# Optimization experiments

Measured on AMD Instinct MI355X. Metric: run time of the kernel, lower is better.

## Reference

```python
import jax, jax.numpy as jnp
import numpy as np

NEG = -9e15
EPS = 1e-5

def setup_inputs() -> dict:
    key = jax.random.key(0)
    k1, k2, k3, k4 = jax.random.split(key, 4)
    B, S, D = 4, 2048, 1024
    q = jax.random.normal(k1, (B, S, D), dtype=jnp.float32)
    k = jax.random.normal(k2, (B, S, D), dtype=jnp.float32)
    v = jax.random.normal(k3, (B, S, D), dtype=jnp.float32)
    mask = jax.random.randint(k4, (B, S, S), 0, 2, dtype=jnp.int32)
    gamma = jnp.ones((D,), dtype=jnp.float32)
    beta = jnp.zeros((D,), dtype=jnp.float32)
    return {"q": q, "k": k, "v": v, "mask": mask, "gamma": gamma, "beta": beta}

def reference(q, k, v, mask, gamma, beta):
    d_k = q.shape[-1]
    # scaled dot-product attention: [B,S,S] logits materialized as in original
    logits = jnp.einsum('bsd,btd->bst', q, k) / jnp.sqrt(jnp.asarray(d_k, q.dtype))
    logits = jnp.where(mask == 0, jnp.asarray(NEG, logits.dtype), logits)
    attn = jax.nn.softmax(logits, axis=-1)
    x = jnp.einsum('bst,btd->bsd', attn, v)
    # dropout is identity at inference; LayerNorm over last dim
    mu = jnp.mean(x, axis=-1, keepdims=True)
    var = jnp.mean(jnp.square(x - mu), axis=-1, keepdims=True)
    xhat = (x - mu) * jax.lax.rsqrt(var + EPS)
    return xhat * gamma + beta
```

## Files before the change

kernel.cpp:

```cpp
#include <hip/hip_runtime.h>
#include <hip/hip_bf16.h>

typedef unsigned short u16;
typedef __attribute__((ext_vector_type(8))) short bf16x8;
typedef __attribute__((ext_vector_type(4))) float f32x4;
typedef __attribute__((ext_vector_type(4))) float float4v;
typedef __attribute__((ext_vector_type(4))) short short4v;

#define BB 4
#define SS 2048
#define DD 1024

__device__ __forceinline__ u16 f2bf(float x){
    unsigned u = __float_as_uint(x);
    return (u16)((u + 0x7fffu + ((u >> 16) & 1u)) >> 16);
}

#define GLD16(g, l) __builtin_amdgcn_global_load_lds( \
    (const __attribute__((address_space(1))) unsigned int*)(g), \
    (__attribute__((address_space(3))) unsigned int*)(l), 16, 0, 0)

__global__ void conv_bf16_kernel(const float* __restrict__ in,
                                 u16* __restrict__ out, int n4, float scale){
    int i = blockIdx.x * 256 + threadIdx.x;
    if (i >= n4) return;
    float4v v = ((const float4v*)in)[i];
    short4v o;
    o[0] = (short)f2bf(v[0] * scale); o[1] = (short)f2bf(v[1] * scale);
    o[2] = (short)f2bf(v[2] * scale); o[3] = (short)f2bf(v[3] * scale);
    ((short4v*)out)[i] = o;
}

__global__ void transpose_v_kernel(const float* __restrict__ v,
                                   u16* __restrict__ vt){
    __shared__ float tile[64][65];
    const int b  = blockIdx.z;
    const int s0 = blockIdx.x << 6;
    const int d0 = blockIdx.y << 6;
    const int tx = threadIdx.x & 15;
    const int ty = threadIdx.x >> 4;
#pragma unroll
    for (int kk = 0; kk < 4; ++kk){
        const float* p = v + ((b * SS + s0 + ty + 16 * kk) * DD) + d0 + tx * 4;
        float4v val = *(const float4v*)p;
        tile[ty + 16 * kk][tx * 4 + 0] = val[0];
        tile[ty + 16 * kk][tx * 4 + 1] = val[1];
        tile[ty + 16 * kk][tx * 4 + 2] = val[2];
        tile[ty + 16 * kk][tx * 4 + 3] = val[3];
    }
    __syncthreads();
#pragma unroll
    for (int kk = 0; kk < 4; ++kk){
        int dy = ty + 16 * kk;
        short4v o;
        o[0] = (short)f2bf(tile[tx * 4 + 0][dy]);
        o[1] = (short)f2bf(tile[tx * 4 + 1][dy]);
        o[2] = (short)f2bf(tile[tx * 4 + 2][dy]);
        o[3] = (short)f2bf(tile[tx * 4 + 3][dy]);
        *(short4v*)&vt[((b * DD + d0 + dy) * SS) + s0 + tx * 4] = o;
    }
}

__global__ void zero_f32(float* __restrict__ p, int n){
    int i = blockIdx.x * 256 + threadIdx.x;
    if (i < n) p[i] = 0.f;
}

__global__ __launch_bounds__(256, 4) void qk_kernel(
    const u16* __restrict__ Qb, const u16* __restrict__ Kb,
    const int* __restrict__ mask, u16* __restrict__ P,
    float* __restrict__ rowsum)
{
    __shared__ __align__(16) u16 Abuf[2][128 * 32];
    __shared__ __align__(16) u16 Bbuf[2][128 * 32];
    __shared__ float rsred[2][128];

    const int flat = blockIdx.x;
    const int swz  = (flat & 7) * 128 + (flat >> 3);
    const int bx = swz & 15, by = (swz >> 4) & 15, b = swz >> 8;

    const int tid  = threadIdx.x;
    const int wid  = tid >> 6, lane = tid & 63;
    const int l16  = lane & 15, g4 = lane >> 4;
    const int wr   = wid >> 1,  wc = wid & 1;
    const int row0 = bx << 7;
    const int col0 = by << 7;

    f32x4 acc[4][4];
    const f32x4 z4 = {0.f, 0.f, 0.f, 0.f};
#pragma unroll
    for (int i = 0; i < 4; ++i)
#pragma unroll
        for (int j = 0; j < 4; ++j) acc[i][j] = z4;

    const int off0 = wid * 1024 + lane * 16;
    const int ar0  = off0 >> 6;
    const int ac0  = (off0 & 63) >> 1;
    const int ldso = wid * 1024 + lane * 16;

    const u16* gQ = Qb + ((size_t)(b * SS + row0 + ar0)) * DD + ac0;
    const u16* gK = Kb + ((size_t)(b * SS + col0 + ar0)) * DD + ac0;

#define QK_STAGE(t, bi) { \
    GLD16(gQ + (t) * 32,            (char*)Abuf[bi] + ldso); \
    GLD16(gQ + 64 * DD + (t) * 32,  (char*)Abuf[bi] + 4096 + ldso); \
    GLD16(gK + (t) * 32,            (char*)Bbuf[bi] + ldso); \
    GLD16(gK + 64 * DD + (t) * 32,  (char*)Bbuf[bi] + 4096 + ldso); }

    QK_STAGE(0, 0);
    __syncthreads();

    const int NT = DD / 32;
    for (int t = 0; t < NT; ++t){
        const int cur = t & 1;
        if (t + 1 < NT) QK_STAGE(t + 1, cur ^ 1);
        bf16x8 af[4], bfr[4];
#pragma unroll
        for (int i = 0; i < 4; ++i){
            af[i]  = *(const bf16x8*)&Abuf[cur][(wr * 64 + i * 16 + l16) * 32 + g4 * 8];
            bfr[i] = *(const bf16x8*)&Bbuf[cur][(wc * 64 + i * 16 + l16) * 32 + g4 * 8];
        }
#pragma unroll
        for (int i = 0; i < 4; ++i)
#pragma unroll
            for (int j = 0; j < 4; ++j)
                acc[i][j] = __builtin_amdgcn_mfma_f32_16x16x32_bf16(af[i], bfr[j], acc[i][j], 0, 0, 0);
        __syncthreads();
    }
#undef QK_STAGE

    float rs[4][4];
#pragma unroll
    for (int i = 0; i < 4; ++i)
#pragma unroll
        for (int r = 0; r < 4; ++r) rs[i][r] = 0.f;

#pragma unroll
    for (int i = 0; i < 4; ++i){
#pragma unroll
        for (int j = 0; j < 4; ++j){
#pragma unroll
            for (int r = 0; r < 4; ++r){
                const int grow = row0 + wr * 64 + i * 16 + g4 * 4 + r;
                const int gcol = col0 + wc * 64 + j * 16 + l16;
                const size_t idx = ((size_t)(b * SS + grow)) * SS + gcol;
                int m = mask[idx];
                float e = m ? __expf(acc[i][j][r]) : 0.f;
                P[idx] = f2bf(e);
                rs[i][r] += e;
            }
        }
    }
#pragma unroll
    for (int i = 0; i < 4; ++i)
#pragma unroll
        for (int r = 0; r < 4; ++r){
            float v = rs[i][r];
            v += __shfl_xor(v, 1); v += __shfl_xor(v, 2);
            v += __shfl_xor(v, 4); v += __shfl_xor(v, 8);
            if (l16 == 0) rsred[wc][wr * 64 + i * 16 + g4 * 4 + r] = v;
        }
    __syncthreads();
    if (tid < 128)
        atomicAdd(&rowsum[b * SS + row0 + tid], rsred[0][tid] + rsred[1][tid]);
}

__global__ __launch_bounds__(256, 4) void pv_kernel(
    const u16* __restrict__ P, const u16* __restrict__ Vt,
    const float* __restrict__ rowsum, u16* __restrict__ Xn)
{
    __shared__ __align__(16) u16 Abuf[2][128 * 32];
    __shared__ __align__(16) u16 Bbuf[2][128 * 32];

    const int flat = blockIdx.x;
    const int swz  = (flat & 7) * 64 + (flat >> 3);
    const int bx = swz & 15, by = (swz >> 4) & 7, b = swz >> 7;

    const int tid  = threadIdx.x;
    const int wid  = tid >> 6, lane = tid & 63;
    const int l16  = lane & 15, g4 = lane >> 4;
    const int wr   = wid >> 1,  wc = wid & 1;
    const int row0 = bx << 7;
    const int col0 = by << 7;

    f32x4 acc[4][4];
    const f32x4 z4 = {0.f, 0.f, 0.f, 0.f};
#pragma unroll
    for (int i = 0; i < 4; ++i)
#pragma unroll
        for (int j = 0; j < 4; ++j) acc[i][j] = z4;

    const int off0 = wid * 1024 + lane * 16;
    const int ar0  = off0 >> 6;
    const int ac0  = (off0 & 63) >> 1;
    const int ldso = wid * 1024 + lane * 16;

    const u16* gP = P  + ((size_t)(b * SS + row0 + ar0)) * SS + ac0;
    const u16* gV = Vt + ((size_t)(b * DD + col0 + ar0)) * SS + ac0;

#define PV_STAGE(t, bi) { \
    GLD16(gP + (t) * 32,            (char*)Abuf[bi] + ldso); \
    GLD16(gP + 64 * SS + (t) * 32,  (char*)Abuf[bi] + 4096 + ldso); \
    GLD16(gV + (t) * 32,            (char*)Bbuf[bi] + ldso); \
    GLD16(gV + 64 * SS + (t) * 32,  (char*)Bbuf[bi] + 4096 + ldso); }

    PV_STAGE(0, 0);
    __syncthreads();

    const int NT = SS / 32;
    for (int t = 0; t < NT; ++t){
        const int cur = t & 1;
        if (t + 1 < NT) PV_STAGE(t + 1, cur ^ 1);
        bf16x8 af[4], bfr[4];
#pragma unroll
        for (int i = 0; i < 4; ++i){
            af[i]  = *(const bf16x8*)&Abuf[cur][(wr * 64 + i * 16 + l16) * 32 + g4 * 8];
            bfr[i] = *(const bf16x8*)&Bbuf[cur][(wc * 64 + i * 16 + l16) * 32 + g4 * 8];
        }
#pragma unroll
        for (int i = 0; i < 4; ++i)
#pragma unroll
            for (int j = 0; j < 4; ++j)
                acc[i][j] = __builtin_amdgcn_mfma_f32_16x16x32_bf16(af[i], bfr[j], acc[i][j], 0, 0, 0);
        __syncthreads();
    }
#undef PV_STAGE

#pragma unroll
    for (int i = 0; i < 4; ++i){
        float inv[4];
#pragma unroll
        for (int r = 0; r < 4; ++r)
            inv[r] = 1.f / rowsum[b * SS + row0 + wr * 64 + i * 16 + g4 * 4 + r];
#pragma unroll
        for (int j = 0; j < 4; ++j){
#pragma unroll
            for (int r = 0; r < 4; ++r){
                const int grow = row0 + wr * 64 + i * 16 + g4 * 4 + r;
                const int gcol = col0 + wc * 64 + j * 16 + l16;
                Xn[((size_t)(b * SS + grow)) * DD + gcol] = f2bf(acc[i][j][r] * inv[r]);
            }
        }
    }
}

__global__ __launch_bounds__(256) void ln_kernel(
    const u16* __restrict__ Xn, const float* __restrict__ gamma,
    const float* __restrict__ beta, float* __restrict__ out)
{
    __shared__ float red[2][4];
    const int row = blockIdx.x;
    const int t = threadIdx.x;
    short4v xv = *(const short4v*)&Xn[(size_t)row * DD + t * 4];
    float x[4];
#pragma unroll
    for (int j = 0; j < 4; ++j)
        x[j] = __uint_as_float(((unsigned)(u16)xv[j]) << 16);
    float s  = x[0] + x[1] + x[2] + x[3];
    float sq = x[0]*x[0] + x[1]*x[1] + x[2]*x[2] + x[3]*x[3];
#pragma unroll
    for (int d = 1; d < 64; d <<= 1){ s += __shfl_xor(s, d); sq += __shfl_xor(sq, d); }
    const int wv = t >> 6;
    if ((t & 63) == 0){ red[0][wv] = s; red[1][wv] = sq; }
    __syncthreads();
    float S  = red[0][0] + red[0][1] + red[0][2] + red[0][3];
    float Sq = red[1][0] + red[1][1] + red[1][2] + red[1][3];
    float mu = S * (1.f / 1024.f);
    float var = Sq * (1.f / 1024.f) - mu * mu;
    float rstd = rsqrtf(var + 1e-5f);
    float4v g  = *(const float4v*)&gamma[t * 4];
    float4v be = *(const float4v*)&beta[t * 4];
    float4v o;
#pragma unroll
    for (int j = 0; j < 4; ++j) o[j] = (x[j] - mu) * rstd * g[j] + be[j];
    *(float4v*)&out[(size_t)row * DD + t * 4] = o;
}

extern "C" void kernel_launch(void* const* d_in, const int* in_sizes, int n_in,
                              void* d_out, int out_size, void* d_ws, size_t ws_size,
                              hipStream_t stream) {
    const float* q     = (const float*)d_in[0];
    const float* k     = (const float*)d_in[1];
    const float* v     = (const float*)d_in[2];
    const int*   mask  = (const int*)d_in[3];
    const float* gamma = (const float*)d_in[4];
    const float* beta  = (const float*)d_in[5];
    float* out = (float*)d_out;

    u16* Qb = (u16*)d_ws;
    u16* Kb = Qb + (size_t)BB * SS * DD;
    u16* Vt = Kb + (size_t)BB * SS * DD;
    u16* P  = Vt + (size_t)BB * SS * DD;
    u16* Xn = P  + (size_t)BB * SS * SS;
    float* rowsum = (float*)(Xn + (size_t)BB * SS * DD);

    const int n4 = BB * SS * DD / 4;
    conv_bf16_kernel<<<n4 / 256, 256, 0, stream>>>(q, Qb, n4, 0.03125f);
    conv_bf16_kernel<<<n4 / 256, 256, 0, stream>>>(k, Kb, n4, 1.0f);
    transpose_v_kernel<<<dim3(SS / 64, DD / 64, BB), 256, 0, stream>>>(v, Vt);
    zero_f32<<<BB * SS / 256, 256, 0, stream>>>(rowsum, BB * SS);

    qk_kernel<<<BB * 16 * 16, 256, 0, stream>>>(Qb, Kb, mask, P, rowsum);
    pv_kernel<<<BB * 16 * 8, 256, 0, stream>>>(P, Vt, rowsum, Xn);
    ln_kernel<<<BB * SS, 256, 0, stream>>>(Xn, gamma, beta, out);
}
```

Baseline: 162.7 us.

## Prefetch mask as bitmasks in QK loop; retile PV kernel to 128x256 with swizzled LDS

In the QK kernel, mask loads are spread across the K-loop iterations and packed into per-row 64-bit ballot bitmasks in LDS, so the epilogue no longer issues scattered int mask reads after the GEMM. The PV kernel moves to 512-thread blocks with 128x256 tiles, a 64-wide K step, XOR-swizzled LDS layout, explicit vmcnt waits and raw barriers, and s_setprio phases around the MFMA groups. The aim is to hide global latency behind compute and raise operand reuse. The cost is more LDS per block, lower occupancy, and fragile hand-written synchronisation.

```diff
diff --git a/kernel.cpp b/kernel.cpp
--- a/kernel.cpp
+++ b/kernel.cpp
@@ -19,6 +19,10 @@
 #define GLD16(g, l) __builtin_amdgcn_global_load_lds( \
     (const __attribute__((address_space(1))) unsigned int*)(g), \
     (__attribute__((address_space(3))) unsigned int*)(l), 16, 0, 0)
+
+#define SCHED0() __builtin_amdgcn_sched_barrier(0)
+#define PH_PRE()  SCHED0(); __builtin_amdgcn_s_barrier(); SCHED0(); __builtin_amdgcn_s_setprio(1)
+#define PH_POST() __builtin_amdgcn_s_setprio(0); SCHED0(); __builtin_amdgcn_s_barrier(); SCHED0()
 
 __global__ void conv_bf16_kernel(const float* __restrict__ in,
                                  u16* __restrict__ out, int n4, float scale){
@@ -68,11 +72,12 @@
 
 __global__ __launch_bounds__(256, 4) void qk_kernel(
     const u16* __restrict__ Qb, const u16* __restrict__ Kb,
-    const int* __restrict__ mask, u16* __restrict__ P,
+    const int* __restrict__ maskg, u16* __restrict__ P,
     float* __restrict__ rowsum)
 {
     __shared__ __align__(16) u16 Abuf[2][128 * 32];
     __shared__ __align__(16) u16 Bbuf[2][128 * 32];
+    __shared__ unsigned long long maskbits[256];
     __shared__ float rsred[2][128];
 
     const int flat = blockIdx.x;
@@ -85,6 +90,7 @@
     const int wr   = wid >> 1,  wc = wid & 1;
     const int row0 = bx << 7;
     const int col0 = by << 7;
+    const int mrowbase = b * SS + row0;
 
     f32x4 acc[4][4];
     const f32x4 z4 = {0.f, 0.f, 0.f, 0.f};
@@ -96,7 +102,7 @@
     const int off0 = wid * 1024 + lane * 16;
     const int ar0  = off0 >> 6;
     const int ac0  = (off0 & 63) >> 1;
-    const int ldso = wid * 1024 + lane * 16;
+    const int ldso = off0;
 
     const u16* gQ = Qb + ((size_t)(b * SS + row0 + ar0)) * DD + ac0;
     const u16* gK = Kb + ((size_t)(b * SS + col0 + ar0)) * DD + ac0;
@@ -108,12 +114,21 @@
     GLD16(gK + 64 * DD + (t) * 32,  (char*)Bbuf[bi] + 4096 + ldso); }
 
     QK_STAGE(0, 0);
-    __syncthreads();
+    asm volatile("s_waitcnt vmcnt(0)" ::: "memory");
+    SCHED0(); __builtin_amdgcn_s_barrier(); SCHED0();
 
     const int NT = DD / 32;
+#pragma unroll 1
     for (int t = 0; t < NT; ++t){
         const int cur = t & 1;
+        const int slot0 = t * 8 + wid * 2;
+        const int mf0 = slot0 * 64 + lane;
+        const int mf1 = mf0 + 64;
+        int mi0 = maskg[(size_t)(mrowbase + (mf0 >> 7)) * SS + col0 + (mf0 & 127)];
+        int mi1 = maskg[(size_t)(mrowbase + (mf1 >> 7)) * SS + col0 + (mf1 & 127)];
+        SCHED0();
         if (t + 1 < NT) QK_STAGE(t + 1, cur ^ 1);
+
         bf16x8 af[4], bfr[4];
 #pragma unroll
         for (int i = 0; i < 4; ++i){
@@ -125,10 +140,20 @@
 #pragma unroll
             for (int j = 0; j < 4; ++j)
                 acc[i][j] = __builtin_amdgcn_mfma_f32_16x16x32_bf16(af[i], bfr[j], acc[i][j], 0, 0, 0);
-        __syncthreads();
+
+        unsigned long long b0 = __ballot(mi0 != 0);
+        unsigned long long b1 = __ballot(mi1 != 0);
+        if (lane == 0){ maskbits[slot0] = b0; maskbits[slot0 + 1] = b1; }
+
+        SCHED0();
+        asm volatile("s_waitcnt vmcnt(0)" ::: "memory");
+        __builtin_amdgcn_s_barrier();
+        SCHED0();
     }
 #undef QK_STAGE
 
+    __syncthreads();
+
     float rs[4][4];
 #pragma unroll
     for (int i = 0; i < 4; ++i)
@@ -139,13 +164,14 @@
     for (int i = 0; i < 4; ++i){
 #pragma unroll
         for (int j = 0; j < 4; ++j){
+            const int gc = wc * 64 + j * 16 + l16;
 #pragma unroll
             for (int r = 0; r < 4; ++r){
-                const int grow = row0 + wr * 64 + i * 16 + g4 * 4 + r;
-                const int gcol = col0 + wc * 64 + j * 16 + l16;
-                const size_t idx = ((size_t)(b * SS + grow)) * SS + gcol;
-                int m = mask[idx];
-                float e = m ? __expf(acc[i][j][r]) : 0.f;
+                const int gr = wr * 64 + i * 16 + g4 * 4 + r;
+                unsigned long long w64 = maskbits[gr * 2 + (gc >> 6)];
+                int keep = (int)((w64 >> (gc & 63)) & 1ull);
+                float e = keep ? __expf(acc[i][j][r]) : 0.f;
+                const size_t idx = (size_t)(mrowbase + gr) * SS + col0 + gc;
                 P[idx] = f2bf(e);
                 rs[i][r] += e;
             }
@@ -165,23 +191,36 @@
         atomicAdd(&rowsum[b * SS + row0 + tid], rsred[0][tid] + rsred[1][tid]);
 }
 
-__global__ __launch_bounds__(256, 4) void pv_kernel(
+__global__ __launch_bounds__(512, 2) void pv_kernel(
     const u16* __restrict__ P, const u16* __restrict__ Vt,
     const float* __restrict__ rowsum, u16* __restrict__ Xn)
 {
-    __shared__ __align__(16) u16 Abuf[2][128 * 32];
-    __shared__ __align__(16) u16 Bbuf[2][128 * 32];
-
-    const int flat = blockIdx.x;
-    const int swz  = (flat & 7) * 64 + (flat >> 3);
-    const int bx = swz & 15, by = (swz >> 4) & 7, b = swz >> 7;
-
-    const int tid  = threadIdx.x;
-    const int wid  = tid >> 6, lane = tid & 63;
-    const int l16  = lane & 15, g4 = lane >> 4;
-    const int wr   = wid >> 1,  wc = wid & 1;
-    const int row0 = bx << 7;
-    const int col0 = by << 7;
+    __shared__ __align__(16) u16 As[2][128 * 64];
+    __shared__ __align__(16) u16 Bs[2][256 * 64];
+
+    const int swz = ((blockIdx.x & 7) << 5) + (blockIdx.x >> 3);
+    const int b   = swz >> 6;
+    const int bx  = (swz >> 2) & 15;
+    const int by  = swz & 3;
+    const int row0 = bx << 7, col0 = by << 8;
+
+    const int tid = threadIdx.x;
+    const int wid = tid >> 6, lane = tid & 63;
+    const int l16 = lane & 15, g4 = lane >> 4;
+    const int wr = wid >> 2, wc = wid & 3;
+
+    const int sr   = tid >> 3;
+    const int scol = ((tid & 7) ^ (sr & 7)) << 3;
+    const u16* gA = P  + (size_t)(b * SS + row0 + sr) * SS + scol;
+    const u16* gB = Vt + (size_t)(b * DD + col0 + sr) * SS + scol;
+    char* const lA0 = (char*)As[0] + tid * 16;
+    char* const lB0 = (char*)Bs[0] + tid * 16;
+    char* const lA1 = (char*)As[1] + tid * 16;
+    char* const lB1 = (char*)Bs[1] + tid * 16;
+
+    const int aRow = (wr * 64 + l16) << 7;
+    const int bRow = (wc * 64 + l16) << 7;
+    const int cx0  = (g4 << 4) ^ ((l16 & 7) << 4);
 
     f32x4 acc[4][4];
     const f32x4 z4 = {0.f, 0.f, 0.f, 0.f};
@@ -190,55 +229,89 @@
 #pragma unroll
         for (int j = 0; j < 4; ++j) acc[i][j] = z4;
 
-    const int off0 = wid * 1024 + lane * 16;
-    const int ar0  = off0 >> 6;
-    const int ac0  = (off0 & 63) >> 1;
-    const int ldso = wid * 1024 + lane * 16;
-
-    const u16* gP = P  + ((size_t)(b * SS + row0 + ar0)) * SS + ac0;
-    const u16* gV = Vt + ((size_t)(b * DD + col0 + ar0)) * SS + ac0;
-
-#define PV_STAGE(t, bi) { \
-    GLD16(gP + (t) * 32,            (char*)Abuf[bi] + ldso); \
-    GLD16(gP + 64 * SS + (t) * 32,  (char*)Abuf[bi] + 4096 + ldso); \
-    GLD16(gV + (t) * 32,            (char*)Bbuf[bi] + ldso); \
-    GLD16(gV + 64 * SS + (t) * 32,  (char*)Bbuf[bi] + 4096 + ldso); }
-
-    PV_STAGE(0, 0);
-    __syncthreads();
-
-    const int NT = SS / 32;
-    for (int t = 0; t < NT; ++t){
-        const int cur = t & 1;
-        if (t + 1 < NT) PV_STAGE(t + 1, cur ^ 1);
-        bf16x8 af[4], bfr[4];
-#pragma unroll
-        for (int i = 0; i < 4; ++i){
-            af[i]  = *(const bf16x8*)&Abuf[cur][(wr * 64 + i * 16 + l16) * 32 + g4 * 8];
-            bfr[i] = *(const bf16x8*)&Bbuf[cur][(wc * 64 + i * 16 + l16) * 32 + g4 * 8];
-        }
-#pragma unroll
-        for (int i = 0; i < 4; ++i)
-#pragma unroll
-            for (int j = 0; j < 4; ++j)
-                acc[i][j] = __builtin_amdgcn_mfma_f32_16x16x32_bf16(af[i], bfr[j], acc[i][j], 0, 0, 0);
-        __syncthreads();
-    }
-#undef PV_STAGE
-
-#pragma unroll
-    for (int i = 0; i < 4; ++i){
+#define STAGE_PV(kt, la, lb) { \
+    const u16* ga_ = gA + (kt) * 64; \
+    const u16* gb_ = gB + (kt) * 64; \
+    GLD16(ga_,            (la)); \
+    GLD16(ga_ +  64 * SS, (la) + 8192); \
+    GLD16(gb_,            (lb)); \
+    GLD16(gb_ +  64 * SS, (lb) + 8192); \
+    GLD16(gb_ + 128 * SS, (lb) + 16384); \
+    GLD16(gb_ + 192 * SS, (lb) + 24576); }
+
+#define LDA2(Ab_, mh, kx) { \
+    const char* p_ = (const char*)(Ab_) + aRow + (mh) * 4096 + ((kx) ? (cx0 ^ 64) : cx0); \
+    fa0 = *(const bf16x8*)(p_); \
+    fa1 = *(const bf16x8*)(p_ + 2048); }
+
+#define LDB4(Bb_, kx) { \
+    const char* p_ = (const char*)(Bb_) + bRow + ((kx) ? (cx0 ^ 64) : cx0); \
+    fb0 = *(const bf16x8*)(p_); \
+    fb1 = *(const bf16x8*)(p_ + 2048); \
+    fb2 = *(const bf16x8*)(p_ + 4096); \
+    fb3 = *(const bf16x8*)(p_ + 6144); }
+
+#define MROWP(mi, fa) \
+    acc[mi][0] = __builtin_amdgcn_mfma_f32_16x16x32_bf16(fa, fb0, acc[mi][0],0,0,0); \
+    acc[mi][1] = __builtin_amdgcn_mfma_f32_16x16x32_bf16(fa, fb1, acc[mi][1],0,0,0); \
+    acc[mi][2] = __builtin_amdgcn_mfma_f32_16x16x32_bf16(fa, fb2, acc[mi][2],0,0,0); \
+    acc[mi][3] = __builtin_amdgcn_mfma_f32_16x16x32_bf16(fa, fb3, acc[mi][3],0,0,0);
+
+    STAGE_PV(0, lA0, lB0);
+    STAGE_PV(1, lA1, lB1);
+    asm volatile("s_waitcnt vmcnt(6)" ::: "memory");
+    SCHED0(); __builtin_amdgcn_s_barrier(); SCHED0();
+
+#pragma unroll 1
+    for (int it = 0; it < 16; ++it){
+        bf16x8 fa0, fa1, fb0, fb1, fb2, fb3;
+        LDA2(As[0], 0, 0); LDB4(Bs[0], 0);
+        PH_PRE(); MROWP(0,fa0) MROWP(1,fa1) PH_POST();
+        LDA2(As[0], 1, 0);
+        PH_PRE(); MROWP(2,fa0) MROWP(3,fa1) PH_POST();
+        LDA2(As[0], 0, 1); LDB4(Bs[0], 1);
+        PH_PRE(); MROWP(0,fa0) MROWP(1,fa1) PH_POST();
+        LDA2(As[0], 1, 1);
+        PH_PRE(); MROWP(2,fa0) MROWP(3,fa1) PH_POST();
+        if (it < 15){
+            STAGE_PV(2*it+2, lA0, lB0);
+            asm volatile("s_waitcnt vmcnt(6)" ::: "memory");
+        } else {
+            asm volatile("s_waitcnt vmcnt(0)" ::: "memory");
+        }
+        SCHED0(); __builtin_amdgcn_s_barrier(); SCHED0();
+        LDA2(As[1], 0, 0); LDB4(Bs[1], 0);
+        PH_PRE(); MROWP(0,fa0) MROWP(1,fa1) PH_POST();
+        LDA2(As[1], 1, 0);
+        PH_PRE(); MROWP(2,fa0) MROWP(3,fa1) PH_POST();
+        LDA2(As[1], 0, 1); LDB4(Bs[1], 1);
+        PH_PRE(); MROWP(0,fa0) MROWP(1,fa1) PH_POST();
+        LDA2(As[1], 1, 1);
+        PH_PRE(); MROWP(2,fa0) MROWP(3,fa1) PH_POST();
+        if (it < 15){
+            STAGE_PV(2*it+3, lA1, lB1);
+            asm volatile("s_waitcnt vmcnt(6)" ::: "memory");
+            SCHED0(); __builtin_amdgcn_s_barrier(); SCHED0();
+        }
+    }
+#undef STAGE_PV
+#undef LDA2
+#undef LDB4
+#undef MROWP
+
+#pragma unroll
+    for (int m = 0; m < 4; ++m){
         float inv[4];
 #pragma unroll
         for (int r = 0; r < 4; ++r)
-            inv[r] = 1.f / rowsum[b * SS + row0 + wr * 64 + i * 16 + g4 * 4 + r];
-#pragma unroll
-        for (int j = 0; j < 4; ++j){
+            inv[r] = 1.f / rowsum[b * SS + row0 + wr * 64 + m * 16 + g4 * 4 + r];
+#pragma unroll
+        for (int n = 0; n < 4; ++n){
+            const int gcol = col0 + wc * 64 + n * 16 + l16;
 #pragma unroll
             for (int r = 0; r < 4; ++r){
-                const int grow = row0 + wr * 64 + i * 16 + g4 * 4 + r;
-                const int gcol = col0 + wc * 64 + j * 16 + l16;
-                Xn[((size_t)(b * SS + grow)) * DD + gcol] = f2bf(acc[i][j][r] * inv[r]);
+                const int grow = row0 + wr * 64 + m * 16 + g4 * 4 + r;
+                Xn[(size_t)(b * SS + grow) * DD + gcol] = f2bf(acc[m][n][r] * inv[r]);
             }
         }
     }
@@ -301,6 +374,6 @@
     zero_f32<<<BB * SS / 256, 256, 0, stream>>>(rowsum, BB * SS);
 
     qk_kernel<<<BB * 16 * 16, 256, 0, stream>>>(Qb, Kb, mask, P, rowsum);
-    pv_kernel<<<BB * 16 * 8, 256, 0, stream>>>(P, Vt, rowsum, Xn);
+    pv_kernel<<<256, 512, 0, stream>>>(P, Vt, rowsum, Xn);
     ln_kernel<<<BB * SS, 256, 0, stream>>>(Xn, gamma, beta, out);
 }
```

Result: no change. 163.0 us (+0.2%).
